# Performance work log

Hardware: AMD Instinct MI355X
Metric: run time of the kernel (lower is better)

Reference implementation:

```python
import jax, jax.numpy as jnp
import numpy as np

VOCAB = 50000
DIM = 768


def setup_inputs() -> dict:
    key = jax.random.key(0)
    k1, k2, k3, k4 = jax.random.split(key, 4)
    token = jax.random.randint(k1, (32, 512), 0, VOCAB, dtype=jnp.int64)
    need_mapper = jax.random.randint(k2, (VOCAB,), 0, 2, dtype=jnp.int32)
    bert_embedding = jax.random.normal(k3, (VOCAB, DIM), dtype=jnp.float32)
    mapper_w = jax.random.normal(k4, (DIM, DIM), dtype=jnp.float32) * (1.0 / np.sqrt(DIM))
    mapper_b = jnp.zeros((DIM,), dtype=jnp.float32)
    return {
        "token": token,
        "need_mapper": need_mapper,
        "bert_embedding": bert_embedding,
        "mapper_w": mapper_w,
        "mapper_b": mapper_b,
    }


def reference(token, need_mapper, bert_embedding, mapper_w, mapper_b):
    # Gather: [B, S, D] -- irregular access into the embedding table.
    vecs = bert_embedding[token]
    # Conditional mapper (vectorized over all tokens; selected by per-id mask).
    mapped = jnp.einsum("bsd,de->bse", vecs, mapper_w) + mapper_b
    need = need_mapper[token].astype(bool)  # [B, S]
    return jnp.where(need[..., None], mapped, vecs)
```

## Files before the change

### kernel.cpp

```cpp
#include <hip/hip_runtime.h>
#include <hip/hip_bf16.h>
#include <stdint.h>
#include <stddef.h>

#define DIM 768

typedef short short8 __attribute__((ext_vector_type(8)));
typedef float f32x4 __attribute__((ext_vector_type(4)));

__device__ inline unsigned short f2bf_rne(float f) {
    union { float f; unsigned u; } x; x.f = f;
    unsigned r = x.u + 0x7fffu + ((x.u >> 16) & 1u);
    return (unsigned short)(r >> 16);
}

__device__ inline void gload_lds16(const void* g, void* l) {
    __builtin_amdgcn_global_load_lds((const __attribute__((address_space(1))) void*)g,
                                     (__attribute__((address_space(3))) void*)l, 16, 0, 0);
}

#define NWBLK 144
__global__ __launch_bounds__(256) void prep_kernel(
    const int* __restrict__ token,
    const int* __restrict__ need_mapper,
    const float* __restrict__ emb,
    const float* __restrict__ w,
    float* __restrict__ out,
    unsigned short* __restrict__ Abf,
    unsigned short* __restrict__ Bt,
    int* __restrict__ flags)
{
    const int tid = threadIdx.x;
    if (blockIdx.x < NWBLK) {
        __shared__ unsigned short t[64][65];
        const int k0 = (blockIdx.x / 12) * 64, n0 = (blockIdx.x % 12) * 64;
#pragma unroll
        for (int p = 0; p < 16; ++p) {
            int e = p * 256 + tid;
            int r = e >> 6, c = e & 63;
            t[c][r] = f2bf_rne(w[(size_t)(k0 + r) * DIM + n0 + c]);
        }
        __syncthreads();
#pragma unroll
        for (int p = 0; p < 16; ++p) {
            int e = p * 256 + tid;
            int r = e >> 6, c = e & 63;
            Bt[(size_t)(n0 + r) * DIM + k0 + c] = t[r][c];
        }
        return;
    }
    int e = (blockIdx.x - NWBLK) * 256 + tid;
    int r = e / 96;
    int q = e - r * 96;
    int tok = token[r];
    int need = need_mapper[tok];
    const float* src = emb + (size_t)tok * DIM + q * 8;
    float4 v0 = *(const float4*)src;
    float4 v1 = *(const float4*)(src + 4);
    unsigned u0 = __float_as_uint(v0.x) + 0x8000u;
    unsigned u1 = __float_as_uint(v0.y) + 0x8000u;
    unsigned u2 = __float_as_uint(v0.z) + 0x8000u;
    unsigned u3 = __float_as_uint(v0.w) + 0x8000u;
    unsigned u4 = __float_as_uint(v1.x) + 0x8000u;
    unsigned u5 = __float_as_uint(v1.y) + 0x8000u;
    unsigned u6 = __float_as_uint(v1.z) + 0x8000u;
    unsigned u7 = __float_as_uint(v1.w) + 0x8000u;
    union { int i4[4]; short8 s; } pk;
    pk.i4[0] = __builtin_amdgcn_perm(u1, u0, 0x07060302);
    pk.i4[1] = __builtin_amdgcn_perm(u3, u2, 0x07060302);
    pk.i4[2] = __builtin_amdgcn_perm(u5, u4, 0x07060302);
    pk.i4[3] = __builtin_amdgcn_perm(u7, u6, 0x07060302);
    *(short8*)(Abf + (size_t)r * DIM + q * 8) = pk.s;
    if (!need) {
        float* dst = out + (size_t)r * DIM + q * 8;
        *(float4*)dst = v0;
        *(float4*)(dst + 4) = v1;
    }
    if (q == 0) flags[r] = need;
}

__global__ __launch_bounds__(256) void gemm_kernel(
    const unsigned short* __restrict__ A,
    const unsigned short* __restrict__ Bt,
    const float* __restrict__ bias,
    const int* __restrict__ flags,
    float* __restrict__ out)
{
    __shared__ unsigned short As[128 * 32];
    __shared__ unsigned short Bs[128 * 32];

    const int tid  = threadIdx.x;
    const int wave = tid >> 6;
    const int lane = tid & 63;
    const int quad = lane >> 4;
    const int l15  = lane & 15;
    const int wm   = wave >> 1;
    const int wn   = wave & 1;
    const int tile_n = blockIdx.x;
    const int tile_m = blockIdx.y;

    const int srow = tid >> 2;
    const int schk = (tid & 3) ^ ((srow >> 1) & 3);
    const unsigned short* Ag = A  + (size_t)(tile_m * 128 + srow) * DIM + schk * 8;
    const unsigned short* Bg = Bt + (size_t)(tile_n * 128 + srow) * DIM + schk * 8;

    unsigned short* AsW = As + wave * 512;
    unsigned short* BsW = Bs + wave * 512;

    const int slot = quad ^ ((l15 >> 1) & 3);

    f32x4 acc[4][4] = {};

    for (int kk = 0; kk < DIM; kk += 32) {
        __syncthreads();
        gload_lds16(Ag + kk,            AsW);
        gload_lds16(Ag + kk + 64 * DIM, AsW + 2048);
        gload_lds16(Bg + kk,            BsW);
        gload_lds16(Bg + kk + 64 * DIM, BsW + 2048);
        __syncthreads();

        short8 af[4], bf[4];
#pragma unroll
        for (int i = 0; i < 4; ++i)
            af[i] = *(const short8*)(As + (wm * 64 + i * 16 + l15) * 32 + slot * 8);
#pragma unroll
        for (int j = 0; j < 4; ++j)
            bf[j] = *(const short8*)(Bs + (wn * 64 + j * 16 + l15) * 32 + slot * 8);
#pragma unroll
        for (int i = 0; i < 4; ++i)
#pragma unroll
            for (int j = 0; j < 4; ++j)
                acc[i][j] = __builtin_amdgcn_mfma_f32_16x16x32_bf16(af[i], bf[j], acc[i][j], 0, 0, 0);
    }

    const int colg = tile_n * 128 + wn * 64 + l15;
    float bv[4];
#pragma unroll
    for (int j = 0; j < 4; ++j) bv[j] = bias[colg + j * 16];

    const int row0 = tile_m * 128 + wm * 64 + quad * 4;
#pragma unroll
    for (int i = 0; i < 4; ++i) {
#pragma unroll
        for (int r = 0; r < 4; ++r) {
            int gm = row0 + i * 16 + r;
            if (flags[gm] != 0) {
                float* orow = out + (size_t)gm * DIM + colg;
#pragma unroll
                for (int j = 0; j < 4; ++j)
                    orow[j * 16] = acc[i][j][r] + bv[j];
            }
        }
    }
}

extern "C" void kernel_launch(void* const* d_in, const int* in_sizes, int n_in,
                              void* d_out, int out_size, void* d_ws, size_t ws_size,
                              hipStream_t stream)
{
    const int*   token       = (const int*)d_in[0];
    const int*   need_mapper = (const int*)d_in[1];
    const float* emb         = (const float*)d_in[2];
    const float* w           = (const float*)d_in[3];
    const float* bias        = (const float*)d_in[4];
    float* out = (float*)d_out;

    const int ntok = in_sizes[0];

    unsigned short* Abf = (unsigned short*)d_ws;
    unsigned short* Bt  = (unsigned short*)((char*)d_ws + (size_t)ntok * DIM * 2);
    int* flags = (int*)((char*)d_ws + (size_t)ntok * DIM * 2 + (size_t)DIM * DIM * 2);

    int gblocks = NWBLK + (ntok * (DIM / 8)) / 256;
    prep_kernel<<<dim3(gblocks), dim3(256), 0, stream>>>(
        token, need_mapper, emb, w, out, Abf, Bt, flags);
    gemm_kernel<<<dim3(DIM / 128, ntok / 128), dim3(256), 0, stream>>>(
        Abf, Bt, bias, flags, out);
}
```

Baseline: 252.5 us.

## Compact mapper-needed rows so GEMM only processes tokens requiring projection

The prep kernel now uses one wave per token and atomically appends rows that need the mapper into a compacted bf16 A matrix, recording a row map. Rows that don't need it are written straight to the output. The GEMM reads the live count, exits early for tiles past it, and scatters results through the row map. This removes roughly half the GEMM work for random masks. The cost is an extra memset, an atomic per block, and dropping the LDS swizzle, which may add bank conflicts.

```diff
diff --git a/kernel.cpp b/kernel.cpp
--- a/kernel.cpp
+++ b/kernel.cpp
@@ -19,73 +19,93 @@
                                      (__attribute__((address_space(3))) void*)l, 16, 0, 0);
 }
 
-#define NWBLK 144
-__global__ __launch_bounds__(256) void prep_kernel(
+__global__ __launch_bounds__(1024) void prep_kernel(
     const int* __restrict__ token,
     const int* __restrict__ need_mapper,
     const float* __restrict__ emb,
     const float* __restrict__ w,
     float* __restrict__ out,
-    unsigned short* __restrict__ Abf,
+    unsigned short* __restrict__ Acmp,
     unsigned short* __restrict__ Bt,
-    int* __restrict__ flags)
+    int* __restrict__ rowmap,
+    int* __restrict__ cnt,
+    int nGatherBlk)
 {
     const int tid = threadIdx.x;
-    if (blockIdx.x < NWBLK) {
-        __shared__ unsigned short t[64][65];
-        const int k0 = (blockIdx.x / 12) * 64, n0 = (blockIdx.x % 12) * 64;
-#pragma unroll
-        for (int p = 0; p < 16; ++p) {
-            int e = p * 256 + tid;
-            int r = e >> 6, c = e & 63;
-            t[c][r] = f2bf_rne(w[(size_t)(k0 + r) * DIM + n0 + c]);
+    if ((int)blockIdx.x < nGatherBlk) {
+        __shared__ int sneed[16], soffs[16], sbase;
+        const int wave = tid >> 6, lane = tid & 63;
+        const int r = blockIdx.x * 16 + wave;
+        const int tok = token[r];
+        const int need = need_mapper[tok];
+        if (lane == 0) sneed[wave] = need;
+
+        const float* src = emb + (size_t)tok * DIM;
+        float4 v[3];
+#pragma unroll
+        for (int j = 0; j < 3; ++j)
+            v[j] = *(const float4*)(src + (j * 64 + lane) * 4);
+
+        __syncthreads();
+        if (tid == 0) {
+            int tot = 0;
+#pragma unroll
+            for (int i = 0; i < 16; ++i) { soffs[i] = tot; tot += sneed[i]; }
+            sbase = atomicAdd(cnt, tot);
         }
         __syncthreads();
-#pragma unroll
-        for (int p = 0; p < 16; ++p) {
-            int e = p * 256 + tid;
-            int r = e >> 6, c = e & 63;
-            Bt[(size_t)(n0 + r) * DIM + k0 + c] = t[r][c];
+
+        if (need) {
+            const int pos = sbase + soffs[wave];
+            if (lane == 0) rowmap[pos] = r;
+            unsigned short* arow = Acmp + (size_t)pos * DIM;
+#pragma unroll
+            for (int j = 0; j < 3; ++j) {
+                ushort4 h;
+                h.x = f2bf_rne(v[j].x); h.y = f2bf_rne(v[j].y);
+                h.z = f2bf_rne(v[j].z); h.w = f2bf_rne(v[j].w);
+                *(ushort4*)(arow + (j * 64 + lane) * 4) = h;
+            }
+        } else {
+            float* drow = out + (size_t)r * DIM;
+#pragma unroll
+            for (int j = 0; j < 3; ++j)
+                *(float4*)(drow + (j * 64 + lane) * 4) = v[j];
         }
         return;
     }
-    int e = (blockIdx.x - NWBLK) * 256 + tid;
-    int r = e / 96;
-    int q = e - r * 96;
-    int tok = token[r];
-    int need = need_mapper[tok];
-    const float* src = emb + (size_t)tok * DIM + q * 8;
-    float4 v0 = *(const float4*)src;
-    float4 v1 = *(const float4*)(src + 4);
-    unsigned u0 = __float_as_uint(v0.x) + 0x8000u;
-    unsigned u1 = __float_as_uint(v0.y) + 0x8000u;
-    unsigned u2 = __float_as_uint(v0.z) + 0x8000u;
-    unsigned u3 = __float_as_uint(v0.w) + 0x8000u;
-    unsigned u4 = __float_as_uint(v1.x) + 0x8000u;
-    unsigned u5 = __float_as_uint(v1.y) + 0x8000u;
-    unsigned u6 = __float_as_uint(v1.z) + 0x8000u;
-    unsigned u7 = __float_as_uint(v1.w) + 0x8000u;
-    union { int i4[4]; short8 s; } pk;
-    pk.i4[0] = __builtin_amdgcn_perm(u1, u0, 0x07060302);
-    pk.i4[1] = __builtin_amdgcn_perm(u3, u2, 0x07060302);
-    pk.i4[2] = __builtin_amdgcn_perm(u5, u4, 0x07060302);
-    pk.i4[3] = __builtin_amdgcn_perm(u7, u6, 0x07060302);
-    *(short8*)(Abf + (size_t)r * DIM + q * 8) = pk.s;
-    if (!need) {
-        float* dst = out + (size_t)r * DIM + q * 8;
-        *(float4*)dst = v0;
-        *(float4*)(dst + 4) = v1;
-    }
-    if (q == 0) flags[r] = need;
+
+    __shared__ unsigned short t[64][65];
+    const int b = blockIdx.x - nGatherBlk;
+    const int k0 = (b / 12) * 64, n0 = (b % 12) * 64;
+#pragma unroll
+    for (int p = 0; p < 4; ++p) {
+        int e = p * 1024 + tid;
+        int r = e >> 6, c = e & 63;
+        t[c][r] = f2bf_rne(w[(size_t)(k0 + r) * DIM + n0 + c]);
+    }
+    __syncthreads();
+#pragma unroll
+    for (int p = 0; p < 4; ++p) {
+        int e = p * 1024 + tid;
+        int r = e >> 6, c = e & 63;
+        Bt[(size_t)(n0 + r) * DIM + k0 + c] = t[r][c];
+    }
 }
 
 __global__ __launch_bounds__(256) void gemm_kernel(
     const unsigned short* __restrict__ A,
     const unsigned short* __restrict__ Bt,
     const float* __restrict__ bias,
-    const int* __restrict__ flags,
+    const int* __restrict__ rowmap,
+    const int* __restrict__ cnt,
     float* __restrict__ out)
 {
+    const int Mp = *cnt;
+    const int tile_n = blockIdx.x;
+    const int tile_m = blockIdx.y;
+    if (tile_m * 128 >= Mp) return;
+
     __shared__ unsigned short As[128 * 32];
     __shared__ unsigned short Bs[128 * 32];
 
@@ -96,18 +116,14 @@
     const int l15  = lane & 15;
     const int wm   = wave >> 1;
     const int wn   = wave & 1;
-    const int tile_n = blockIdx.x;
-    const int tile_m = blockIdx.y;
 
     const int srow = tid >> 2;
-    const int schk = (tid & 3) ^ ((srow >> 1) & 3);
-    const unsigned short* Ag = A  + (size_t)(tile_m * 128 + srow) * DIM + schk * 8;
-    const unsigned short* Bg = Bt + (size_t)(tile_n * 128 + srow) * DIM + schk * 8;
+    const int schk = (tid & 3) * 8;
+    const unsigned short* Ag = A  + (size_t)(tile_m * 128 + srow) * DIM + schk;
+    const unsigned short* Bg = Bt + (size_t)(tile_n * 128 + srow) * DIM + schk;
 
     unsigned short* AsW = As + wave * 512;
     unsigned short* BsW = Bs + wave * 512;
-
-    const int slot = quad ^ ((l15 >> 1) & 3);
 
     f32x4 acc[4][4] = {};
 
@@ -122,10 +138,10 @@
         short8 af[4], bf[4];
 #pragma unroll
         for (int i = 0; i < 4; ++i)
-            af[i] = *(const short8*)(As + (wm * 64 + i * 16 + l15) * 32 + slot * 8);
+            af[i] = *(const short8*)(As + (wm * 64 + i * 16 + l15) * 32 + quad * 8);
 #pragma unroll
         for (int j = 0; j < 4; ++j)
-            bf[j] = *(const short8*)(Bs + (wn * 64 + j * 16 + l15) * 32 + slot * 8);
+            bf[j] = *(const short8*)(Bs + (wn * 64 + j * 16 + l15) * 32 + quad * 8);
 #pragma unroll
         for (int i = 0; i < 4; ++i)
 #pragma unroll
@@ -144,8 +160,8 @@
 #pragma unroll
         for (int r = 0; r < 4; ++r) {
             int gm = row0 + i * 16 + r;
-            if (flags[gm] != 0) {
-                float* orow = out + (size_t)gm * DIM + colg;
+            if (gm < Mp) {
+                float* orow = out + (size_t)rowmap[gm] * DIM + colg;
 #pragma unroll
                 for (int j = 0; j < 4; ++j)
                     orow[j * 16] = acc[i][j][r] + bv[j];
@@ -167,13 +183,18 @@
 
     const int ntok = in_sizes[0];
 
-    unsigned short* Abf = (unsigned short*)d_ws;
-    unsigned short* Bt  = (unsigned short*)((char*)d_ws + (size_t)ntok * DIM * 2);
-    int* flags = (int*)((char*)d_ws + (size_t)ntok * DIM * 2 + (size_t)DIM * DIM * 2);
-
-    int gblocks = NWBLK + (ntok * (DIM / 8)) / 256;
-    prep_kernel<<<dim3(gblocks), dim3(256), 0, stream>>>(
-        token, need_mapper, emb, w, out, Abf, Bt, flags);
+    const size_t ACMP_B  = (size_t)ntok * DIM * 2;
+    const size_t BT_B    = (size_t)DIM * DIM * 2;
+    unsigned short* Acmp = (unsigned short*)d_ws;
+    unsigned short* Bt   = (unsigned short*)((char*)d_ws + ACMP_B);
+    int* rowmap          = (int*)((char*)d_ws + ACMP_B + BT_B);
+    int* cnt             = (int*)((char*)d_ws + ACMP_B + BT_B + (size_t)ntok * 4);
+
+    hipMemsetAsync(cnt, 0, 4, stream);
+
+    const int nGatherBlk = ntok / 16;
+    prep_kernel<<<dim3(nGatherBlk + 144), dim3(1024), 0, stream>>>(
+        token, need_mapper, emb, w, out, Acmp, Bt, rowmap, cnt, nGatherBlk);
     gemm_kernel<<<dim3(DIM / 128, ntok / 128), dim3(256), 0, stream>>>(
-        Abf, Bt, bias, flags, out);
-}
+        Acmp, Bt, bias, rowmap, cnt, out);
+}
```

After: 245.2 us. -2.9%, faster.
